# Performance work log

Hardware: AMD Instinct MI355X
Metric: run time of the kernel (lower is better)

Reference implementation:

```python
import jax, jax.numpy as jnp
import numpy as np

D_MODEL = 1024
N_HEADS = 16
D_HEAD = D_MODEL // N_HEADS


def setup_inputs() -> dict:
    key = jax.random.key(0)
    k1, k2, k3 = jax.random.split(key, 3)
    x = jax.random.normal(k1, (4, 2048, D_MODEL), dtype=jnp.float32)
    # torch Linear(d, 3d, bias=False): y = x @ W.T with W [3d, d].
    # We store the transposed form W_qkv [d, 3d] so y = x @ W_qkv (same math).
    scale = 1.0 / np.sqrt(D_MODEL)
    W_qkv = jax.random.normal(k2, (D_MODEL, 3 * D_MODEL), dtype=jnp.float32) * scale
    W_o = jax.random.normal(k3, (D_MODEL, D_MODEL), dtype=jnp.float32) * scale
    return {"x": x, "W_qkv": W_qkv, "W_o": W_o}


def reference(x, W_qkv, W_o):
    B, T, C = x.shape
    qkv = x @ W_qkv                              # [B, T, 3C]
    Q, K, V = jnp.split(qkv, 3, axis=-1)
    def to_heads(t):
        return t.reshape(B, T, N_HEADS, D_HEAD).transpose(0, 2, 1, 3)  # [B,H,T,d]
    Q, K, V = to_heads(Q), to_heads(K), to_heads(V)
    scores = jnp.einsum("bhqd,bhkd->bhqk", Q, K) / np.sqrt(D_HEAD)
    attn = jax.nn.softmax(scores, axis=-1)
    # dropout is identity in eval/deterministic mode
    context = jnp.einsum("bhqk,bhkd->bhqd", attn, V)
    context = context.transpose(0, 2, 1, 3).reshape(B, T, C)
    return context @ W_o
```

## Files before the change

kernel.cpp:

```cpp
#include <hip/hip_runtime.h>
#include <hip/hip_bf16.h>

typedef __attribute__((ext_vector_type(8))) short short8;
typedef __attribute__((ext_vector_type(4))) float f32x4;
typedef __attribute__((ext_vector_type(16))) float f32x16;
typedef __attribute__((ext_vector_type(2))) unsigned int uint2v;
typedef __attribute__((ext_vector_type(4))) unsigned int uint4v;

#define SEQ    2048
#define DM     1024
#define NH     16
#define DH     64
#define NBATCH 4
#define MTOK   (NBATCH * SEQ)
#define SEG    ((size_t)NBATCH * NH * SEQ * DH)
#define QSCALE 0.18033688f

static __device__ __forceinline__ unsigned bfbits(float f) {
  unsigned u = __float_as_uint(f);
  return u + 0x7fffu + ((u >> 16) & 1u);
}
static __device__ __forceinline__ unsigned short f2bf(float f) {
  return (unsigned short)(bfbits(f) >> 16);
}
static __device__ __forceinline__ unsigned pack2bf(float lo, float hi) {
  return __builtin_amdgcn_perm(bfbits(hi), bfbits(lo), 0x07060302u);
}
static __device__ __forceinline__ unsigned pack2tr(unsigned ulo, unsigned uhi) {
  return __builtin_amdgcn_perm(uhi, ulo, 0x07060302u);
}

typedef const __attribute__((address_space(1))) unsigned int* gp_t;
typedef __attribute__((address_space(3))) unsigned int* lp_t;
static __device__ __forceinline__ void gload_lds16(const void* g, void* l) {
  __builtin_amdgcn_global_load_lds((gp_t)g, (lp_t)l, 16, 0, 0);
}

__global__ __launch_bounds__(256) void xcast(const float* __restrict__ x,
                                             unsigned short* __restrict__ xb) {
  size_t i = ((size_t)blockIdx.x * 256 + threadIdx.x) * 8;
  f32x4 a = *(const f32x4*)&x[i];
  f32x4 b = *(const f32x4*)&x[i + 4];
  uint4v s;
  s[0] = pack2bf(a[0], a[1]);
  s[1] = pack2bf(a[2], a[3]);
  s[2] = pack2bf(b[0], b[1]);
  s[3] = pack2bf(b[2], b[3]);
  *(uint4v*)&xb[i] = s;
}

__global__ __launch_bounds__(256) void transpose_w(
    const float* __restrict__ W, unsigned short* __restrict__ WT, int K, int N) {
  __shared__ float T[64][65];
  const int tid = threadIdx.x;
  const int n0 = blockIdx.x * 64;
  const int k0 = blockIdx.y * 64;
#pragma unroll
  for (int it = 0; it < 4; it++) {
    int row = it * 16 + (tid >> 4);
    int c4 = (tid & 15) * 4;
    f32x4 v = *(const f32x4*)&W[(size_t)(k0 + row) * N + n0 + c4];
#pragma unroll
    for (int j = 0; j < 4; j++) T[row][c4 + j] = v[j];
  }
  __syncthreads();
#pragma unroll
  for (int it = 0; it < 2; it++) {
    int chunk = tid + it * 256;
    int n = chunk >> 3;
    int c8 = (chunk & 7) * 8;
    uint4v s;
#pragma unroll
    for (int j = 0; j < 4; j++)
      s[j] = pack2bf(T[c8 + 2 * j][n], T[c8 + 2 * j + 1][n]);
    *(uint4v*)&WT[(size_t)(n0 + n) * K + k0 + c8] = s;
  }
}

template <int MODE>
__global__ __launch_bounds__(256) void gemm_kernel(
    const void* __restrict__ Av, const unsigned short* __restrict__ BT,
    unsigned short* __restrict__ out0, unsigned short* __restrict__ out1,
    unsigned short* __restrict__ out2, float* __restrict__ outf,
    int M, int N, int K) {
  __shared__ unsigned short As[128][64];
  __shared__ unsigned short Bs[128][64];

  const int tid = threadIdx.x;
  const int wave = tid >> 6;
  const int lane = tid & 63;
  const int quad = lane >> 4;
  const int lc = lane & 15;
  const int wr = wave >> 1;
  const int wc = wave & 1;
  const int m0 = blockIdx.y * 128;
  const int n0 = blockIdx.x * 128;
  const int xsw = lc & 7;
  const int lr8 = lane >> 3;
  const int sgo = ((lane & 7) ^ (lr8 & 7)) * 8;

  f32x4 acc[4][4];
#pragma unroll
  for (int i = 0; i < 4; i++)
#pragma unroll
    for (int j = 0; j < 4; j++) acc[i][j] = (f32x4){0.f, 0.f, 0.f, 0.f};

  for (int k0 = 0; k0 < K; k0 += 64) {
    if (MODE == 0) {
      const float* A = (const float*)Av;
#pragma unroll
      for (int i = 0; i < 4; i++) {
        int chunk = tid + i * 256;
        int r = chunk >> 3;
        int g = chunk & 7;
        int scol = (g ^ (r & 7)) * 8;
        f32x4 v0 = *(const f32x4*)&A[(size_t)(m0 + r) * K + k0 + scol];
        f32x4 v1 = *(const f32x4*)&A[(size_t)(m0 + r) * K + k0 + scol + 4];
        uint4v s;
        s[0] = pack2bf(v0[0], v0[1]);
        s[1] = pack2bf(v0[2], v0[3]);
        s[2] = pack2bf(v1[0], v1[1]);
        s[3] = pack2bf(v1[2], v1[3]);
        *(uint4v*)&As[r][g * 8] = s;
      }
    } else {
      const unsigned short* A = (const unsigned short*)Av;
#pragma unroll
      for (int it = 0; it < 4; it++) {
        int rbase = wave * 32 + it * 8;
        gload_lds16(&A[(size_t)(m0 + rbase + lr8) * K + k0 + sgo],
                    &As[rbase][0]);
      }
    }
#pragma unroll
    for (int it = 0; it < 4; it++) {
      int rbase = wave * 32 + it * 8;
      gload_lds16(&BT[(size_t)(n0 + rbase + lr8) * K + k0 + sgo],
                  &Bs[rbase][0]);
    }
    __syncthreads();

#pragma unroll
    for (int kc = 0; kc < 2; kc++) {
      short8 aA[4], bB[4];
#pragma unroll
      for (int mt = 0; mt < 4; mt++)
        aA[mt] = *(const short8*)&As[wr * 64 + mt * 16 + lc]
                                    [((kc * 4 + quad) ^ xsw) * 8];
#pragma unroll
      for (int nt = 0; nt < 4; nt++)
        bB[nt] = *(const short8*)&Bs[wc * 64 + nt * 16 + lc]
                                    [((kc * 4 + quad) ^ xsw) * 8];
#pragma unroll
      for (int mt = 0; mt < 4; mt++)
#pragma unroll
        for (int nt = 0; nt < 4; nt++)
          acc[mt][nt] = __builtin_amdgcn_mfma_f32_16x16x32_bf16(
              aA[mt], bB[nt], acc[mt][nt], 0, 0, 0);
    }
    __syncthreads();
  }

  const int c = n0 >> 10;
#pragma unroll
  for (int mt = 0; mt < 4; mt++)
#pragma unroll
    for (int nt = 0; nt < 4; nt++) {
      int rb = m0 + wr * 64 + mt * 16 + quad * 4;
      int col = n0 + wc * 64 + nt * 16 + lc;
      if (MODE == 1) {
#pragma unroll
        for (int r = 0; r < 4; r++)
          outf[(size_t)(rb + r) * N + col] = acc[mt][nt][r];
      } else {
        int rem = col & 1023;
        int h = rem >> 6;
        int dd = rem & 63;
        int b = rb >> 11;
        int tt = rb & 2047;
        if (c == 2) {
          uint2v pk;
          pk[0] = pack2bf(acc[mt][nt][0], acc[mt][nt][1]);
          pk[1] = pack2bf(acc[mt][nt][2], acc[mt][nt][3]);
          *(uint2v*)&out2[(((size_t)(b * NH + h)) * DH + dd) * SEQ + tt] = pk;
        } else {
          unsigned short* dst = (c == 0) ? out0 : out1;
          float sc = (c == 0) ? QSCALE : 1.0f;
#pragma unroll
          for (int r = 0; r < 4; r++)
            dst[(((size_t)(b * NH + h) * SEQ + tt + r) << 6) + dd] =
                f2bf(acc[mt][nt][r] * sc);
        }
      }
    }
}

__global__ __launch_bounds__(256) void attn_kernel(
    const unsigned short* __restrict__ Q, const unsigned short* __restrict__ K,
    const unsigned short* __restrict__ Vt, unsigned short* __restrict__ ctx) {
  __shared__ unsigned short KsL[2][64 * 64];
  __shared__ unsigned short VtL[2][64 * 64];
  __shared__ float lbuf[4][32];

  const int tid = threadIdx.x;
  const int wave = tid >> 6;
  const int lane = tid & 63;
  const int half = lane >> 5;
  const int l31 = lane & 31;
  const int bh = blockIdx.y;
  const int q0 = blockIdx.x * 128 + wave * 32;
  const size_t kqbase = (size_t)bh * SEQ * DH;
  const size_t vbase = (size_t)bh * DH * SEQ;

  short8 bQ[4];
#pragma unroll
  for (int dc = 0; dc < 4; dc++)
    bQ[dc] = *(const short8*)&Q[kqbase + (size_t)(q0 + l31) * DH + dc * 16 + half * 8];

  f32x16 o[2];
#pragma unroll
  for (int nb = 0; nb < 2; nb++)
#pragma unroll
    for (int j = 0; j < 16; j++) o[nb][j] = 0.f;
  float l_part = 0.f;

  const int xsw = l31 & 7;
  const int g0 = wave * 128 + lane;
  const int r0 = g0 >> 3, r1 = (g0 + 64) >> 3;
  const size_t so0 = (size_t)r0 * DH + (((g0 & 7) ^ (r0 & 7)) * 8);
  const size_t so1 = (size_t)r1 * DH + (((g0 & 7) ^ (r1 & 7)) * 8);
  const size_t sv0 = (size_t)r0 * SEQ + (((g0 & 7) ^ (r0 & 7)) * 8);
  const size_t sv1 = (size_t)r1 * SEQ + (((g0 & 7) ^ (r1 & 7)) * 8);
  const int ldo = wave * 1024;

  auto stage = [&](int kt, int b) {
    const size_t kg = kqbase + (size_t)kt * 64 * DH;
    const size_t vg = vbase + (size_t)kt * 64;
    unsigned short* kd = &KsL[b][ldo];
    unsigned short* vd = &VtL[b][ldo];
    gload_lds16(&K[kg + so0], kd);
    gload_lds16(&K[kg + so1], kd + 512);
    gload_lds16(&Vt[vg + sv0], vd);
    gload_lds16(&Vt[vg + sv1], vd + 512);
  };

  stage(0, 0);
  __syncthreads();

  for (int kt = 0; kt < SEQ / 64; kt++) {
    const int cur = kt & 1;
    if (kt + 1 < SEQ / 64) stage(kt + 1, cur ^ 1);
    const unsigned short* kcur = &KsL[cur][0];
    const unsigned short* vcur = &VtL[cur][0];

#pragma unroll
    for (int kb = 0; kb < 2; kb++) {
      f32x16 s;
#pragma unroll
      for (int j = 0; j < 16; j++) s[j] = 0.f;
      __builtin_amdgcn_s_setprio(1);
#pragma unroll
      for (int dc = 0; dc < 4; dc++) {
        const short8 aK = *(const short8*)&kcur[(size_t)(kb * 32 + l31) * 64 +
                                                ((dc * 2 + half) ^ xsw) * 8];
        s = __builtin_amdgcn_mfma_f32_32x32x16_bf16(aK, bQ[dc], s, 0, 0, 0);
      }
      __builtin_amdgcn_s_setprio(0);

      unsigned d0[4], d1[4];
#pragma unroll
      for (int gq = 0; gq < 4; gq++) {
        unsigned u0 = __float_as_uint(__builtin_amdgcn_exp2f(s[gq * 4 + 0]));
        unsigned u1 = __float_as_uint(__builtin_amdgcn_exp2f(s[gq * 4 + 1]));
        unsigned u2 = __float_as_uint(__builtin_amdgcn_exp2f(s[gq * 4 + 2]));
        unsigned u3 = __float_as_uint(__builtin_amdgcn_exp2f(s[gq * 4 + 3]));
        float t0 = __uint_as_float(u0 & 0xffff0000u);
        float t1 = __uint_as_float(u1 & 0xffff0000u);
        float t2 = __uint_as_float(u2 & 0xffff0000u);
        float t3 = __uint_as_float(u3 & 0xffff0000u);
        l_part += (t0 + t1) + (t2 + t3);
        d0[gq] = pack2tr(u0, u1);
        d1[gq] = pack2tr(u2, u3);
      }

#pragma unroll
      for (int kcl = 0; kcl < 2; kcl++) {
        unsigned w0 = d0[kcl * 2], w2 = d0[kcl * 2 + 1];
        unsigned w1 = d1[kcl * 2], w3 = d1[kcl * 2 + 1];
        asm("v_permlane32_swap_b32 %0, %1" : "+v"(w0), "+v"(w2));
        asm("v_permlane32_swap_b32 %0, %1" : "+v"(w1), "+v"(w3));
        union { unsigned u[4]; short8 s8; } cv;
        cv.u[0] = w0; cv.u[1] = w1; cv.u[2] = w2; cv.u[3] = w3;
        const int kc = kb * 2 + kcl;
        __builtin_amdgcn_s_setprio(1);
#pragma unroll
        for (int nb = 0; nb < 2; nb++) {
          const short8 bV = *(const short8*)&vcur[(size_t)(nb * 32 + l31) * 64 +
                                                  ((kc * 2 + half) ^ xsw) * 8];
          o[nb] = __builtin_amdgcn_mfma_f32_32x32x16_bf16(cv.s8, bV, o[nb], 0, 0, 0);
        }
        __builtin_amdgcn_s_setprio(0);
      }
    }
    __syncthreads();
  }

  l_part += __shfl_xor(l_part, 32);
  lbuf[wave][l31] = 1.0f / l_part;
  __syncthreads();

  const int b = bh >> 4;
  const int h = bh & 15;
#pragma unroll
  for (int gq = 0; gq < 4; gq++)
#pragma unroll
    for (int j = 0; j < 4; j++) {
      int ql = j + gq * 8 + half * 4;
      float inv = lbuf[wave][ql];
      int token = blockIdx.x * 128 + wave * 32 + ql;
#pragma unroll
      for (int nb = 0; nb < 2; nb++)
        ctx[((size_t)b * SEQ + token) * DM + h * DH + nb * 32 + l31] =
            f2bf(o[nb][gq * 4 + j] * inv);
    }
}

extern "C" void kernel_launch(void* const* d_in, const int* in_sizes, int n_in,
                              void* d_out, int out_size, void* d_ws,
                              size_t ws_size, hipStream_t stream) {
  const float* x = (const float*)d_in[0];
  const float* Wqkv = (const float*)d_in[1];
  const float* Wo = (const float*)d_in[2];
  float* out = (float*)d_out;
  unsigned short* ws = (unsigned short*)d_ws;

  unsigned short* Qb = ws;
  unsigned short* Kb = ws + SEG;
  unsigned short* Vt = ws + 2 * SEG;
  unsigned short* Ctx = ws + 3 * SEG;
  unsigned short* WqT = Ctx + (size_t)MTOK * DM;
  unsigned short* WoT = WqT + (size_t)3 * DM * DM;
  unsigned short* Xb = WoT + (size_t)DM * DM;
  const size_t need =
      ((size_t)(Xb - ws) + (size_t)MTOK * DM) * sizeof(unsigned short);

  transpose_w<<<dim3(3 * DM / 64, DM / 64), 256, 0, stream>>>(Wqkv, WqT, DM, 3 * DM);
  transpose_w<<<dim3(DM / 64, DM / 64), 256, 0, stream>>>(Wo, WoT, DM, DM);

  if (ws_size >= need) {
    xcast<<<(MTOK * DM) / (256 * 8), 256, 0, stream>>>(x, Xb);
    gemm_kernel<2><<<dim3(3 * DM / 128, MTOK / 128), 256, 0, stream>>>(
        (const void*)Xb, WqT, Qb, Kb, Vt, nullptr, MTOK, 3 * DM, DM);
  } else {
    gemm_kernel<0><<<dim3(3 * DM / 128, MTOK / 128), 256, 0, stream>>>(
        (const void*)x, WqT, Qb, Kb, Vt, nullptr, MTOK, 3 * DM, DM);
  }
  attn_kernel<<<dim3(SEQ / 128, NBATCH * NH), 256, 0, stream>>>(Qb, Kb, Vt, Ctx);
  gemm_kernel<1><<<dim3(DM / 128, MTOK / 128), 256, 0, stream>>>(
      (const void*)Ctx, WoT, nullptr, nullptr, nullptr, out, MTOK, DM, DM);
}
```

Baseline: 288.9 us.

## Compute softmax row sums via MFMA with ones vector and remap attention grid

The per-row softmax denominator is no longer accumulated with scalar VALU adds, a cross-half shuffle and an LDS buffer. It is now computed by an extra MFMA that multiplies the probability tile by a ones matrix, so it lands in the same accumulator layout as the output. This removes VALU work and a barrier but adds one more MFMA per 16-wide K chunk, 50% more PV MFMAs. The launch also becomes a 1D grid with a remap that places all query tiles of a head on one XCD, meant to improve K/V reuse in L2.

Measured after the change: 283.7 us. About the same (-1.8%).

```diff
diff --git a/kernel.cpp b/kernel.cpp
--- a/kernel.cpp
+++ b/kernel.cpp
@@ -200,15 +200,16 @@
     const unsigned short* __restrict__ Vt, unsigned short* __restrict__ ctx) {
   __shared__ unsigned short KsL[2][64 * 64];
   __shared__ unsigned short VtL[2][64 * 64];
-  __shared__ float lbuf[4][32];
 
   const int tid = threadIdx.x;
   const int wave = tid >> 6;
   const int lane = tid & 63;
   const int half = lane >> 5;
   const int l31 = lane & 31;
-  const int bh = blockIdx.y;
-  const int q0 = blockIdx.x * 128 + wave * 32;
+  const int id = blockIdx.x;
+  const int bh = (id & 7) * 8 + (id >> 3) / 16;
+  const int qt = (id >> 3) & 15;
+  const int q0 = qt * 128 + wave * 32;
   const size_t kqbase = (size_t)bh * SEQ * DH;
   const size_t vbase = (size_t)bh * DH * SEQ;
 
@@ -217,12 +218,22 @@
   for (int dc = 0; dc < 4; dc++)
     bQ[dc] = *(const short8*)&Q[kqbase + (size_t)(q0 + l31) * DH + dc * 16 + half * 8];
 
-  f32x16 o[2];
+  f32x16 o[2], o_l;
 #pragma unroll
   for (int nb = 0; nb < 2; nb++)
 #pragma unroll
     for (int j = 0; j < 16; j++) o[nb][j] = 0.f;
-  float l_part = 0.f;
+#pragma unroll
+  for (int j = 0; j < 16; j++) o_l[j] = 0.f;
+
+  f32x16 zf;
+#pragma unroll
+  for (int j = 0; j < 16; j++) zf[j] = 0.f;
+
+  union { unsigned u[4]; short8 s8; } onesu;
+#pragma unroll
+  for (int j = 0; j < 4; j++) onesu.u[j] = 0x3f803f80u;
+  const short8 ones = onesu.s8;
 
   const int xsw = l31 & 7;
   const int g0 = wave * 128 + lane;
@@ -255,10 +266,8 @@
 
 #pragma unroll
     for (int kb = 0; kb < 2; kb++) {
-      f32x16 s;
-#pragma unroll
-      for (int j = 0; j < 16; j++) s[j] = 0.f;
       __builtin_amdgcn_s_setprio(1);
+      f32x16 s = zf;
 #pragma unroll
       for (int dc = 0; dc < 4; dc++) {
         const short8 aK = *(const short8*)&kcur[(size_t)(kb * 32 + l31) * 64 +
@@ -274,11 +283,6 @@
         unsigned u1 = __float_as_uint(__builtin_amdgcn_exp2f(s[gq * 4 + 1]));
         unsigned u2 = __float_as_uint(__builtin_amdgcn_exp2f(s[gq * 4 + 2]));
         unsigned u3 = __float_as_uint(__builtin_amdgcn_exp2f(s[gq * 4 + 3]));
-        float t0 = __uint_as_float(u0 & 0xffff0000u);
-        float t1 = __uint_as_float(u1 & 0xffff0000u);
-        float t2 = __uint_as_float(u2 & 0xffff0000u);
-        float t3 = __uint_as_float(u3 & 0xffff0000u);
-        l_part += (t0 + t1) + (t2 + t3);
         d0[gq] = pack2tr(u0, u1);
         d1[gq] = pack2tr(u2, u3);
       }
@@ -299,15 +303,12 @@
                                                   ((kc * 2 + half) ^ xsw) * 8];
           o[nb] = __builtin_amdgcn_mfma_f32_32x32x16_bf16(cv.s8, bV, o[nb], 0, 0, 0);
         }
+        o_l = __builtin_amdgcn_mfma_f32_32x32x16_bf16(cv.s8, ones, o_l, 0, 0, 0);
         __builtin_amdgcn_s_setprio(0);
       }
     }
     __syncthreads();
   }
-
-  l_part += __shfl_xor(l_part, 32);
-  lbuf[wave][l31] = 1.0f / l_part;
-  __syncthreads();
 
   const int b = bh >> 4;
   const int h = bh & 15;
@@ -315,13 +316,14 @@
   for (int gq = 0; gq < 4; gq++)
 #pragma unroll
     for (int j = 0; j < 4; j++) {
+      int r = gq * 4 + j;
       int ql = j + gq * 8 + half * 4;
-      float inv = lbuf[wave][ql];
-      int token = blockIdx.x * 128 + wave * 32 + ql;
+      float inv = __builtin_amdgcn_rcpf(o_l[r]);
+      int token = qt * 128 + wave * 32 + ql;
 #pragma unroll
       for (int nb = 0; nb < 2; nb++)
         ctx[((size_t)b * SEQ + token) * DM + h * DH + nb * 32 + l31] =
-            f2bf(o[nb][gq * 4 + j] * inv);
+            f2bf(o[nb][r] * inv);
     }
 }
 
@@ -355,7 +357,7 @@
     gemm_kernel<0><<<dim3(3 * DM / 128, MTOK / 128), 256, 0, stream>>>(
         (const void*)x, WqT, Qb, Kb, Vt, nullptr, MTOK, 3 * DM, DM);
   }
-  attn_kernel<<<dim3(SEQ / 128, NBATCH * NH), 256, 0, stream>>>(Qb, Kb, Vt, Ctx);
+  attn_kernel<<<dim3(SEQ / 128 * NBATCH * NH), 256, 0, stream>>>(Qb, Kb, Vt, Ctx);
   gemm_kernel<1><<<dim3(DM / 128, MTOK / 128), 256, 0, stream>>>(
       (const void*)Ctx, WoT, nullptr, nullptr, nullptr, out, MTOK, DM, DM);
 }
```
